# Kernel tuning notes

Measured on AMD Instinct MI355X. Metric: run time of the kernel, lower is better.

Reference implementation:

```python
import jax, jax.numpy as jnp
import numpy as np

BETA = 0.25

def setup_inputs() -> dict:
    key = jax.random.key(0)
    k1, k2 = jax.random.split(key)
    z = jax.random.normal(k1, (32, 256, 32, 32), dtype=jnp.float32)
    # embedding init ~ U(-1/K, 1/K) as intended by the module
    K, D = 1024, 256
    codebook = jax.random.uniform(k2, (K, D), dtype=jnp.float32, minval=-1.0 / K, maxval=1.0 / K)
    return {"z": z, "codebook": codebook}


def reference(z, codebook):
    # z: [B, D, H, W] -> [B, H, W, D]
    zt = jnp.transpose(z, (0, 2, 3, 1))
    B, H, W, D = zt.shape
    z_flat = zt.reshape(-1, D)  # [N, D]
    # pairwise squared distance: ||z||^2 + ||e||^2 - 2 z e^T
    dist = (
        jnp.sum(z_flat * z_flat, axis=1, keepdims=True)
        + jnp.sum(codebook * codebook, axis=1)[None, :]
        - 2.0 * jnp.matmul(z_flat, codebook.T)
    )  # [N, K]
    idx = jnp.argmin(dist, axis=1)  # [N]
    z_q = codebook[idx].reshape(B, H, W, D)
    sg = jax.lax.stop_gradient
    loss = jnp.mean((sg(z_q) - zt) ** 2) + BETA * jnp.mean((sg(zt) - z_q) ** 2)
    # straight-through estimator
    z_q = zt + sg(z_q - zt)
    z_q = jnp.transpose(z_q, (0, 3, 1, 2))  # back to [B, D, H, W]
    return z_q, idx, loss
```

## Files before the change

kernel.cpp:

```cpp
#include <hip/hip_runtime.h>


#define D_DIM   256
#define K_CODES 1024
#define HW      1024
#define MT      128
#define NT      256
#define BK      16
#define THREADS 512

#define ZQ_OFF   0
#define IDX_OFF  8388608
#define LOSS_OFF 8421376

#define SMEM_FLOATS (D_DIM*MT + BK*NT + MT + MT)
#define SMEM_BYTES  (SMEM_FLOATS * 4)

extern __shared__ float smem[];

__global__ void enorm_kernel(const float* __restrict__ cb, float* __restrict__ enorm) {
    int gt = blockIdx.x * blockDim.x + threadIdx.x;
    int k = gt >> 6;
    int lane = gt & 63;
    const float4* row = (const float4*)(cb + (size_t)k * D_DIM);
    float4 v = row[lane];
    float s = fmaf(v.x, v.x, fmaf(v.y, v.y, fmaf(v.z, v.z, v.w * v.w)));
    #pragma unroll
    for (int off = 32; off; off >>= 1) s += __shfl_xor(s, off);
    if (lane == 0) enorm[k] = s;
}

__global__ __launch_bounds__(THREADS, 2) void vq_kernel(
        const float* __restrict__ z, const float* __restrict__ cb,
        const float* __restrict__ enorm, float* __restrict__ out)
{
    float* As = smem;
    float* Es = smem + D_DIM * MT;
    int*   bestm   = (int*)(smem + D_DIM*MT + BK*NT);
    float* znorm_s = (float*)(smem + D_DIM*MT + BK*NT + MT);

    const int t   = threadIdx.x;
    const int blk = blockIdx.x;
    const int b   = blk >> 3;
    const int p0  = (blk & 7) * MT;
    const float* zb = z + (size_t)b * D_DIM * HW;

    for (int i = t; i < D_DIM * MT / 4; i += THREADS) {
        int d = i >> 5, m4 = i & 31;
        *(float4*)(As + d * MT + m4 * 4) = *(const float4*)(zb + d * HW + p0 + m4 * 4);
    }
    __syncthreads();

    {
        int m = t & (MT - 1), q = t >> 7;
        const float* col = As + m;
        double zp = 0.0;
        #pragma unroll 8
        for (int d = q * 64; d < q * 64 + 64; ++d) {
            double v = (double)col[d * MT];
            zp += v * v;
        }
        double* zscr = (double*)Es;
        zscr[q * MT + m] = zp;
    }
    __syncthreads();
    if (t < MT) {
        double* zscr = (double*)Es;
        double s = (zscr[t] + zscr[MT + t]) + (zscr[2 * MT + t] + zscr[3 * MT + t]);
        znorm_s[t] = (float)s;
    }
    __syncthreads();

    const int tx = t & 31, ty = t >> 5;
    const int m_base = ty * 8;
    const int kx = tx * 8;

    float znf[8];
    #pragma unroll
    for (int i = 0; i < 8; ++i) znf[i] = znorm_s[m_base + i];

    float bestv[8]; int besti[8];
    #pragma unroll
    for (int i = 0; i < 8; ++i) { bestv[i] = 3.4e38f; besti[i] = 0; }

    for (int c = 0; c < 4; ++c) {
        const int k0 = c * NT;
        float acc[8][8];
        #pragma unroll
        for (int i = 0; i < 8; ++i)
            #pragma unroll
            for (int j = 0; j < 8; ++j) acc[i][j] = 0.f;

        for (int dk = 0; dk < D_DIM; dk += BK) {
            __syncthreads();
            for (int i = t; i < BK * NT / 4; i += THREADS) {
                int kk = i >> 2, d4 = i & 3;
                float4 v = *(const float4*)(cb + (size_t)(k0 + kk) * D_DIM + dk + d4 * 4);
                Es[(d4 * 4 + 0) * NT + kk] = v.x;
                Es[(d4 * 4 + 1) * NT + kk] = v.y;
                Es[(d4 * 4 + 2) * NT + kk] = v.z;
                Es[(d4 * 4 + 3) * NT + kk] = v.w;
            }
            __syncthreads();
            #pragma unroll
            for (int dd = 0; dd < BK; ++dd) {
                float a[8], e[8];
                *(float4*)(a)     = *(const float4*)(As + (dk + dd) * MT + m_base);
                *(float4*)(a + 4) = *(const float4*)(As + (dk + dd) * MT + m_base + 4);
                *(float4*)(e)     = *(const float4*)(Es + dd * NT + kx);
                *(float4*)(e + 4) = *(const float4*)(Es + dd * NT + kx + 4);
                #pragma unroll
                for (int i = 0; i < 8; ++i)
                    #pragma unroll
                    for (int j = 0; j < 8; ++j)
                        acc[i][j] = fmaf(a[i], e[j], acc[i][j]);
            }
        }
        #pragma unroll
        for (int j = 0; j < 8; ++j) {
            float bn = enorm[k0 + kx + j];
            int kidx = k0 + kx + j;
            #pragma unroll
            for (int i = 0; i < 8; ++i) {
                float A   = znf[i] + bn;
                float val = A - 2.0f * acc[i][j];
                if (val < bestv[i] || (val == bestv[i] && kidx < besti[i])) {
                    bestv[i] = val; besti[i] = kidx;
                }
            }
        }
    }

    #pragma unroll
    for (int i = 0; i < 8; ++i) {
        float v = bestv[i]; int ix = besti[i];
        #pragma unroll
        for (int off = 16; off; off >>= 1) {
            float ov = __shfl_xor(v, off);
            int   oi = __shfl_xor(ix, off);
            if (ov < v || (ov == v && oi < ix)) { v = ov; ix = oi; }
        }
        if (tx == 0) {
            bestm[m_base + i] = ix;
            out[IDX_OFF + (size_t)blk * MT + m_base + i] = (float)ix;
        }
    }
    __syncthreads();

    float lsum = 0.f;
    const size_t zq_base = (size_t)b * D_DIM * HW + p0;
    for (int i2 = t; i2 < D_DIM * MT / 4; i2 += THREADS) {
        int p = i2 & (MT - 1), d4 = i2 >> 7;
        int idx = bestm[p];
        float4 cv = *(const float4*)(cb + (size_t)idx * D_DIM + d4 * 4);
        float z0 = As[(d4 * 4 + 0) * MT + p];
        float z1 = As[(d4 * 4 + 1) * MT + p];
        float z2 = As[(d4 * 4 + 2) * MT + p];
        float z3 = As[(d4 * 4 + 3) * MT + p];
        float e0 = cv.x - z0, e1 = cv.y - z1, e2 = cv.z - z2, e3 = cv.w - z3;
        lsum = fmaf(e0, e0, lsum); lsum = fmaf(e1, e1, lsum);
        lsum = fmaf(e2, e2, lsum); lsum = fmaf(e3, e3, lsum);
        out[zq_base + (size_t)(d4 * 4 + 0) * HW + p] = cv.x;
        out[zq_base + (size_t)(d4 * 4 + 1) * HW + p] = cv.y;
        out[zq_base + (size_t)(d4 * 4 + 2) * HW + p] = cv.z;
        out[zq_base + (size_t)(d4 * 4 + 3) * HW + p] = cv.w;
    }
    #pragma unroll
    for (int off = 32; off; off >>= 1) lsum += __shfl_xor(lsum, off);
    __syncthreads();
    if ((t & 63) == 0) Es[t >> 6] = lsum;
    __syncthreads();
    if (t == 0) {
        float s = 0.f;
        #pragma unroll
        for (int w = 0; w < 8; ++w) s += Es[w];
        atomicAdd(out + LOSS_OFF, s * (1.25f / 8388608.f));
    }
}

extern "C" void kernel_launch(void* const* d_in, const int* in_sizes, int n_in,
                              void* d_out, int out_size, void* d_ws, size_t ws_size,
                              hipStream_t stream) {
    const float* z  = (const float*)d_in[0];
    const float* cb = (const float*)d_in[1];
    float* out = (float*)d_out;
    float* enorm = (float*)d_ws;

    hipMemsetAsync(out + LOSS_OFF, 0, sizeof(float), stream);

    enorm_kernel<<<256, 256, 0, stream>>>(cb, enorm);

    hipFuncSetAttribute((const void*)vq_kernel,
                        hipFuncAttributeMaxDynamicSharedMemorySize, SMEM_BYTES);
    vq_kernel<<<256, THREADS, SMEM_BYTES, stream>>>(z, cb, enorm, out);
}
```

Baseline: 303.2 us.

## Double-buffer codebook tiles with register prefetch and split column mapping

Replaces the single-buffered codebook staging loop (two barriers per k-step) with a double-buffered shared tile of BK=8. The next tile is prefetched into registers before the FMA block and written to the alternate buffer afterwards, so only one barrier is needed per step. Each thread's eight codebook columns are also split into two groups of four, 128 apart, which changes the LDS read pattern to reduce bank conflicts. The cost is more steps (half-size tiles) and slightly more shared memory.

```diff
diff --git a/kernel.cpp b/kernel.cpp
--- a/kernel.cpp
+++ b/kernel.cpp
@@ -6,14 +6,15 @@
 #define HW      1024
 #define MT      128
 #define NT      256
-#define BK      16
+#define BK      8
 #define THREADS 512
+#define NSTEP   128
 
 #define ZQ_OFF   0
 #define IDX_OFF  8388608
 #define LOSS_OFF 8421376
 
-#define SMEM_FLOATS (D_DIM*MT + BK*NT + MT + MT)
+#define SMEM_FLOATS (D_DIM*MT + 2*BK*NT + MT + MT)
 #define SMEM_BYTES  (SMEM_FLOATS * 4)
 
 extern __shared__ float smem[];
@@ -36,8 +37,8 @@
 {
     float* As = smem;
     float* Es = smem + D_DIM * MT;
-    int*   bestm   = (int*)(smem + D_DIM*MT + BK*NT);
-    float* znorm_s = (float*)(smem + D_DIM*MT + BK*NT + MT);
+    int*   bestm   = (int*)(smem + D_DIM*MT + 2*BK*NT);
+    float* znorm_s = (float*)(smem + D_DIM*MT + 2*BK*NT + MT);
 
     const int t   = threadIdx.x;
     const int blk = blockIdx.x;
@@ -73,7 +74,7 @@
 
     const int tx = t & 31, ty = t >> 5;
     const int m_base = ty * 8;
-    const int kx = tx * 8;
+    const int kx4 = tx * 4;
 
     float znf[8];
     #pragma unroll
@@ -83,6 +84,19 @@
     #pragma unroll
     for (int i = 0; i < 8; ++i) { bestv[i] = 3.4e38f; besti[i] = 0; }
 
+    const int skk = t >> 1, sd4 = t & 1;
+    const float* cbp = cb + (size_t)skk * D_DIM + sd4 * 4;
+
+    {
+        float4 v = *(const float4*)(cbp);
+        Es[(sd4 * 4 + 0) * NT + skk] = v.x;
+        Es[(sd4 * 4 + 1) * NT + skk] = v.y;
+        Es[(sd4 * 4 + 2) * NT + skk] = v.z;
+        Es[(sd4 * 4 + 3) * NT + skk] = v.w;
+    }
+    __syncthreads();
+
+    int cur = 0;
     for (int c = 0; c < 4; ++c) {
         const int k0 = c * NT;
         float acc[8][8];
@@ -91,35 +105,46 @@
             #pragma unroll
             for (int j = 0; j < 8; ++j) acc[i][j] = 0.f;
 
-        for (int dk = 0; dk < D_DIM; dk += BK) {
-            __syncthreads();
-            for (int i = t; i < BK * NT / 4; i += THREADS) {
-                int kk = i >> 2, d4 = i & 3;
-                float4 v = *(const float4*)(cb + (size_t)(k0 + kk) * D_DIM + dk + d4 * 4);
-                Es[(d4 * 4 + 0) * NT + kk] = v.x;
-                Es[(d4 * 4 + 1) * NT + kk] = v.y;
-                Es[(d4 * 4 + 2) * NT + kk] = v.z;
-                Es[(d4 * 4 + 3) * NT + kk] = v.w;
-            }
-            __syncthreads();
+        for (int s = 0; s < 32; ++s) {
+            const int g = c * 32 + s;
+            const bool more = (g + 1 < NSTEP);
+            float4 sv;
+            if (more) {
+                const int gn = g + 1;
+                sv = *(const float4*)(cbp + (((size_t)(gn >> 5)) << 16) + ((gn & 31) << 3));
+            }
+
+            const float* Ec = Es + cur * (BK * NT);
+            const int dk = s * BK;
             #pragma unroll
             for (int dd = 0; dd < BK; ++dd) {
                 float a[8], e[8];
                 *(float4*)(a)     = *(const float4*)(As + (dk + dd) * MT + m_base);
                 *(float4*)(a + 4) = *(const float4*)(As + (dk + dd) * MT + m_base + 4);
-                *(float4*)(e)     = *(const float4*)(Es + dd * NT + kx);
-                *(float4*)(e + 4) = *(const float4*)(Es + dd * NT + kx + 4);
+                *(float4*)(e)     = *(const float4*)(Ec + dd * NT + kx4);
+                *(float4*)(e + 4) = *(const float4*)(Ec + dd * NT + 128 + kx4);
                 #pragma unroll
                 for (int i = 0; i < 8; ++i)
                     #pragma unroll
                     for (int j = 0; j < 8; ++j)
                         acc[i][j] = fmaf(a[i], e[j], acc[i][j]);
             }
-        }
+
+            if (more) {
+                float* En = Es + (cur ^ 1) * (BK * NT);
+                En[(sd4 * 4 + 0) * NT + skk] = sv.x;
+                En[(sd4 * 4 + 1) * NT + skk] = sv.y;
+                En[(sd4 * 4 + 2) * NT + skk] = sv.z;
+                En[(sd4 * 4 + 3) * NT + skk] = sv.w;
+            }
+            __syncthreads();
+            cur ^= 1;
+        }
+
         #pragma unroll
         for (int j = 0; j < 8; ++j) {
-            float bn = enorm[k0 + kx + j];
-            int kidx = k0 + kx + j;
+            const int kidx = k0 + ((j < 4) ? (kx4 + j) : (124 + kx4 + j));
+            const float bn = enorm[kidx];
             #pragma unroll
             for (int i = 0; i < 8; ++i) {
                 float A   = znf[i] + bn;
```

Measured after the change: 295.5 us. 1.03x faster.

## Retile VQ distance GEMM to 64x512 with register-prefetched codebook loads

Applied to the files above, without the earlier changes.

Shrinks the row tile to 64 and widens the code tile to 512, doubling the grid to 512 blocks and raising the launch-bounds occupancy target. Each thread now owns one codebook row and prefetches its next float4 into a register while the current BK=4 slice is consumed, so global loads overlap compute. The trade-off is one barrier pair per 4-wide depth step (128 steps), which adds synchronisation overhead, and the 4-blocks-per-SM target may push the 64-float accumulator tile toward register spills.

```diff
diff --git a/kernel.cpp b/kernel.cpp
--- a/kernel.cpp
+++ b/kernel.cpp
@@ -4,10 +4,11 @@
 #define D_DIM   256
 #define K_CODES 1024
 #define HW      1024
-#define MT      128
-#define NT      256
-#define BK      16
+#define MT      64
+#define NT      512
+#define BK      4
 #define THREADS 512
+#define NSTEP   128
 
 #define ZQ_OFF   0
 #define IDX_OFF  8388608
@@ -30,33 +31,38 @@
     if (lane == 0) enorm[k] = s;
 }
 
-__global__ __launch_bounds__(THREADS, 2) void vq_kernel(
+__global__ __launch_bounds__(THREADS, 4)
+void vq_kernel(
         const float* __restrict__ z, const float* __restrict__ cb,
         const float* __restrict__ enorm, float* __restrict__ out)
 {
     float* As = smem;
     float* Es = smem + D_DIM * MT;
-    int*   bestm   = (int*)(smem + D_DIM*MT + BK*NT);
-    float* znorm_s = (float*)(smem + D_DIM*MT + BK*NT + MT);
+    float* znorm_s = smem + D_DIM * MT + BK * NT;
+    int*   bestm   = (int*)(smem + D_DIM * MT + BK * NT + MT);
 
     const int t   = threadIdx.x;
     const int blk = blockIdx.x;
-    const int b   = blk >> 3;
-    const int p0  = (blk & 7) * MT;
+    const int b   = blk >> 4;
+    const int p0  = (blk & 15) * MT;
     const float* zb = z + (size_t)b * D_DIM * HW;
 
+    const float* cbp = cb + (size_t)t * D_DIM;
+
+    float4 sv = *(const float4*)(cbp);
+
     for (int i = t; i < D_DIM * MT / 4; i += THREADS) {
-        int d = i >> 5, m4 = i & 31;
+        int d = i >> 4, m4 = i & 15;
         *(float4*)(As + d * MT + m4 * 4) = *(const float4*)(zb + d * HW + p0 + m4 * 4);
     }
     __syncthreads();
 
     {
-        int m = t & (MT - 1), q = t >> 7;
+        int m = t & (MT - 1), q = t >> 6;
         const float* col = As + m;
         double zp = 0.0;
         #pragma unroll 8
-        for (int d = q * 64; d < q * 64 + 64; ++d) {
+        for (int d = q * 32; d < q * 32 + 32; ++d) {
             double v = (double)col[d * MT];
             zp += v * v;
         }
@@ -66,68 +72,76 @@
     __syncthreads();
     if (t < MT) {
         double* zscr = (double*)Es;
-        double s = (zscr[t] + zscr[MT + t]) + (zscr[2 * MT + t] + zscr[3 * MT + t]);
+        double s = 0.0;
+        #pragma unroll
+        for (int q = 0; q < 8; ++q) s += zscr[q * MT + t];
         znorm_s[t] = (float)s;
     }
-    __syncthreads();
-
-    const int tx = t & 31, ty = t >> 5;
-    const int m_base = ty * 8;
-    const int kx = tx * 8;
-
-    float znf[8];
-    #pragma unroll
-    for (int i = 0; i < 8; ++i) znf[i] = znorm_s[m_base + i];
+
+    const int tx = t & 63;
+    const int m_base = (t >> 6) * 8;
+    const int kx4 = tx * 4;
 
     float bestv[8]; int besti[8];
     #pragma unroll
     for (int i = 0; i < 8; ++i) { bestv[i] = 3.4e38f; besti[i] = 0; }
 
-    for (int c = 0; c < 4; ++c) {
-        const int k0 = c * NT;
-        float acc[8][8];
-        #pragma unroll
-        for (int i = 0; i < 8; ++i)
+    float acc[8][8];
+    #pragma unroll
+    for (int i = 0; i < 8; ++i)
+        #pragma unroll
+        for (int j = 0; j < 8; ++j) acc[i][j] = 0.f;
+
+    for (int g = 0; g < NSTEP; ++g) {
+        const int c = g >> 6, s = g & 63;
+
+        __syncthreads();
+        Es[0 * NT + t] = sv.x;
+        Es[1 * NT + t] = sv.y;
+        Es[2 * NT + t] = sv.z;
+        Es[3 * NT + t] = sv.w;
+
+        {
+            const int gn = (g < NSTEP - 1) ? g + 1 : NSTEP - 1;
+            sv = *(const float4*)(cbp + (((size_t)(gn >> 6)) << 17) + ((gn & 63) << 2));
+        }
+        __syncthreads();
+
+        const int dk = s * BK;
+        #pragma unroll
+        for (int dd = 0; dd < BK; ++dd) {
+            const float* Ar = As + (dk + dd) * MT + m_base;
+            float a[8], e[8];
+            *(float4*)(a)     = *(const float4*)(Ar);
+            *(float4*)(a + 4) = *(const float4*)(Ar + 4);
+            const float* Er = Es + dd * NT + kx4;
+            *(float4*)(e)     = *(const float4*)(Er);
+            *(float4*)(e + 4) = *(const float4*)(Er + 256);
             #pragma unroll
-            for (int j = 0; j < 8; ++j) acc[i][j] = 0.f;
-
-        for (int dk = 0; dk < D_DIM; dk += BK) {
-            __syncthreads();
-            for (int i = t; i < BK * NT / 4; i += THREADS) {
-                int kk = i >> 2, d4 = i & 3;
-                float4 v = *(const float4*)(cb + (size_t)(k0 + kk) * D_DIM + dk + d4 * 4);
-                Es[(d4 * 4 + 0) * NT + kk] = v.x;
-                Es[(d4 * 4 + 1) * NT + kk] = v.y;
-                Es[(d4 * 4 + 2) * NT + kk] = v.z;
-                Es[(d4 * 4 + 3) * NT + kk] = v.w;
-            }
-            __syncthreads();
+            for (int i = 0; i < 8; ++i)
+                #pragma unroll
+                for (int j = 0; j < 8; ++j)
+                    acc[i][j] = fmaf(a[i], e[j], acc[i][j]);
+        }
+
+        if (s == 63) {
             #pragma unroll
-            for (int dd = 0; dd < BK; ++dd) {
-                float a[8], e[8];
-                *(float4*)(a)     = *(const float4*)(As + (dk + dd) * MT + m_base);
-                *(float4*)(a + 4) = *(const float4*)(As + (dk + dd) * MT + m_base + 4);
-                *(float4*)(e)     = *(const float4*)(Es + dd * NT + kx);
-                *(float4*)(e + 4) = *(const float4*)(Es + dd * NT + kx + 4);
+            for (int j = 0; j < 8; ++j) {
+                const int kidx = c * NT + ((j < 4) ? (kx4 + j) : (252 + kx4 + j));
+                const float bn = enorm[kidx];
                 #pragma unroll
-                for (int i = 0; i < 8; ++i)
-                    #pragma unroll
-                    for (int j = 0; j < 8; ++j)
-                        acc[i][j] = fmaf(a[i], e[j], acc[i][j]);
-            }
-        }
-        #pragma unroll
-        for (int j = 0; j < 8; ++j) {
-            float bn = enorm[k0 + kx + j];
-            int kidx = k0 + kx + j;
-            #pragma unroll
-            for (int i = 0; i < 8; ++i) {
-                float A   = znf[i] + bn;
-                float val = A - 2.0f * acc[i][j];
-                if (val < bestv[i] || (val == bestv[i] && kidx < besti[i])) {
-                    bestv[i] = val; besti[i] = kidx;
+                for (int i = 0; i < 8; ++i) {
+                    float A   = znorm_s[m_base + i] + bn;
+                    float val = A - 2.0f * acc[i][j];
+                    if (val < bestv[i] || (val == bestv[i] && kidx < besti[i])) {
+                        bestv[i] = val; besti[i] = kidx;
+                    }
                 }
             }
+            #pragma unroll
+            for (int i = 0; i < 8; ++i)
+                #pragma unroll
+                for (int j = 0; j < 8; ++j) acc[i][j] = 0.f;
         }
     }
 
@@ -135,7 +149,7 @@
     for (int i = 0; i < 8; ++i) {
         float v = bestv[i]; int ix = besti[i];
         #pragma unroll
-        for (int off = 16; off; off >>= 1) {
+        for (int off = 32; off; off >>= 1) {
             float ov = __shfl_xor(v, off);
             int   oi = __shfl_xor(ix, off);
             if (ov < v || (ov == v && oi < ix)) { v = ov; ix = oi; }
@@ -150,7 +164,7 @@
     float lsum = 0.f;
     const size_t zq_base = (size_t)b * D_DIM * HW + p0;
     for (int i2 = t; i2 < D_DIM * MT / 4; i2 += THREADS) {
-        int p = i2 & (MT - 1), d4 = i2 >> 7;
+        int p = i2 & (MT - 1), d4 = i2 >> 6;
         int idx = bestm[p];
         float4 cv = *(const float4*)(cb + (size_t)idx * D_DIM + d4 * 4);
         float z0 = As[(d4 * 4 + 0) * MT + p];
@@ -192,5 +206,5 @@
 
     hipFuncSetAttribute((const void*)vq_kernel,
                         hipFuncAttributeMaxDynamicSharedMemorySize, SMEM_BYTES);
-    vq_kernel<<<256, THREADS, SMEM_BYTES, stream>>>(z, cb, enorm, out);
+    vq_kernel<<<512, THREADS, SMEM_BYTES, stream>>>(z, cb, enorm, out);
 }
```

Result: slower. 545.5 us (+79.9%).
